# Performance work log

Hardware: AMD Instinct MI355X
Metric: run time of the kernel (lower is better)

## Reference

```python
import jax, jax.numpy as jnp
import numpy as np

HARD_NUM = 700      # hardcoded self.hard_num in HardOIMLoss
OIM_SCALAR = 30.0   # oim_scalar init arg
N, D, P, Q = 4096, 256, 5532, 5000


def _l2norm(x):
    return x / jnp.linalg.norm(x, axis=-1, keepdims=True)


def setup_inputs() -> dict:
    key = jax.random.key(0)
    k1, k2, k3, k4, k5 = jax.random.split(key, 5)
    # OIM features and lookup tables are L2-normalized rows
    inputs = _l2norm(jax.random.normal(k1, (N, D), dtype=jnp.float32))
    lut = _l2norm(jax.random.normal(k2, (P, D), dtype=jnp.float32))
    cq = _l2norm(jax.random.normal(k3, (Q, D), dtype=jnp.float32))
    reliability = jax.random.uniform(k4, (P + Q,), dtype=jnp.float32)
    labels = jax.random.randint(k5, (N,), 0, P, dtype=jnp.int32)
    return {"inputs": inputs, "labels": labels, "lut": lut, "cq": cq,
            "reliability": reliability}


def reference(inputs, labels, lut, cq, reliability):
    # projected[n, c] = <inputs_n, table_c> * reliability_c ;  table = [lut; cq]
    table = jnp.concatenate([lut, cq], axis=0)            # [P+Q, D]
    projected = (inputs @ table.T) * reliability[None, :]  # [N, P+Q]
    C = projected.shape[1]
    # value at sorted-descending index HARD_NUM == (HARD_NUM+1)-th largest
    boundary = jax.lax.top_k(projected, HARD_NUM + 1)[0][:, -1]  # [N]
    hard_mask = projected >= boundary[:, None]
    label_mask = jnp.arange(C, dtype=labels.dtype)[None, :] == labels[:, None]
    mask = hard_mask | label_mask
    logits = jnp.where(mask, projected * OIM_SCALAR, -jnp.inf)
    # cross entropy (mean over rows); label column is always unmasked
    logZ = jax.scipy.special.logsumexp(logits, axis=1)
    tgt = jnp.take_along_axis(logits, labels[:, None].astype(jnp.int32), axis=1)[:, 0]
    return jnp.mean(logZ - tgt)
```

## Files before the change

kernel.cpp:

```cpp
#include <hip/hip_runtime.h>
#include <math.h>

#define N_ROWS 4096
#define DIM    256
#define P_SZ   5532
#define Q_SZ   5000
#define C_COLS 10532
#define TPAD   10624
#define PSTR   10624
#define NGR    (PSTR / 8)
#define K_SEL  701
#define SCALAR 30.0f
#define C2     (SCALAR * 1.4426950408889634f)

typedef __attribute__((ext_vector_type(8))) short   short8;
typedef __attribute__((ext_vector_type(4))) float   float4_t;
typedef __attribute__((ext_vector_type(4))) unsigned short ushort4_t;
typedef __attribute__((ext_vector_type(8))) unsigned short ushort8_t;

__device__ __forceinline__ unsigned short f2bf(float f) {
    unsigned u = __float_as_uint(f);
    unsigned r = u + 0x7FFFu + ((u >> 16) & 1u);
    return (unsigned short)(r >> 16);
}
__device__ __forceinline__ float bf2f(unsigned short u) {
    return __uint_as_float((unsigned)u << 16);
}
__device__ __forceinline__ unsigned key16(unsigned short u) {
    return (u & 0x8000u) ? (unsigned)(~u & 0xFFFFu) : (unsigned)(u | 0x8000u);
}
__device__ __forceinline__ void gload16(const void* g, void* l) {
    __builtin_amdgcn_global_load_lds(
        (const __attribute__((address_space(1))) unsigned int*)g,
        (__attribute__((address_space(3))) unsigned int*)l, 16, 0, 0);
}

#define NIN_G  (N_ROWS * DIM / 4)
#define NTAB_G (TPAD * DIM / 4)

__global__ __launch_bounds__(256) void convert_bf16(
    const float* __restrict__ inputs, const float* __restrict__ lut,
    const float* __restrict__ cq, unsigned short* __restrict__ in_bf,
    unsigned short* __restrict__ tab_bf)
{
    const int g = blockIdx.x * 256 + threadIdx.x;
    if (g >= NIN_G + NTAB_G) return;
    float4_t v;
    unsigned short* dst;
    if (g < NIN_G) {
        v = *(const float4_t*)&inputs[(size_t)g * 4];
        dst = in_bf + (size_t)g * 4;
    } else {
        const int t = g - NIN_G;
        const int row = t >> 6;
        const int c4  = (t & 63) * 4;
        if (row < P_SZ)        v = *(const float4_t*)&lut[(size_t)row * DIM + c4];
        else if (row < C_COLS) v = *(const float4_t*)&cq[(size_t)(row - P_SZ) * DIM + c4];
        else                   v = (float4_t){0.f, 0.f, 0.f, 0.f};
        dst = tab_bf + (size_t)t * 4;
    }
    ushort4_t h = { f2bf(v.x), f2bf(v.y), f2bf(v.z), f2bf(v.w) };
    *(ushort4_t*)dst = h;
}

#define NWG_X 83
#define NWG_Y 32
#define NWG   (NWG_X * NWG_Y)
#define CSTR  132

__global__ __launch_bounds__(256) void gemm_proj(
    const unsigned short* __restrict__ in_bf,
    const unsigned short* __restrict__ tab_bf,
    const float* __restrict__ rel,
    unsigned short* __restrict__ proj)
{
    __shared__ __align__(16) unsigned short smem[128 * CSTR];
    unsigned short* At = smem;
    unsigned short* Bt = smem + 128 * 64;

    const int tid  = threadIdx.x;
    const int lane = tid & 63, wid = tid >> 6;
    const int wm = wid >> 1, wn = wid & 1;

    const int phys = blockIdx.x;
    const int wg   = (phys & 7) * (NWG / 8) + (phys >> 3);
    const int bx   = wg >> 5;
    const int by   = wg & 31;
    const int row0 = by * 128, col0 = bx * 128;

    float4_t acc[4][4];
    #pragma unroll
    for (int i = 0; i < 4; ++i)
        #pragma unroll
        for (int j = 0; j < 4; ++j)
            acc[i][j] = (float4_t){0.f, 0.f, 0.f, 0.f};

    for (int k0 = 0; k0 < DIM; k0 += 64) {
        #pragma unroll
        for (int it = 0; it < 4; ++it) {
            const int g  = it * 256 + tid;
            const int r  = g >> 3;
            const int kb = ((g & 7) * 16) ^ ((r & 7) << 4);
            gload16(in_bf  + (size_t)(row0 + r) * DIM + k0 + (kb >> 1),
                    (char*)At + g * 16);
            gload16(tab_bf + (size_t)(col0 + r) * DIM + k0 + (kb >> 1),
                    (char*)Bt + g * 16);
        }
        __syncthreads();

        #pragma unroll
        for (int kk = 0; kk < 2; ++kk) {
            const int krow = lane & 15;
            const int kb   = kk * 64 + ((lane >> 4) << 4);
            short8 af[4], bfr[4];
            #pragma unroll
            for (int i = 0; i < 4; ++i) {
                const int r = wm * 64 + i * 16 + krow;
                af[i] = *(const short8*)((const char*)At + (r * 128 + (kb ^ ((r & 7) << 4))));
            }
            #pragma unroll
            for (int j = 0; j < 4; ++j) {
                const int r = wn * 64 + j * 16 + krow;
                bfr[j] = *(const short8*)((const char*)Bt + (r * 128 + (kb ^ ((r & 7) << 4))));
            }
            #pragma unroll
            for (int i = 0; i < 4; ++i)
                #pragma unroll
                for (int j = 0; j < 4; ++j)
                    acc[i][j] = __builtin_amdgcn_mfma_f32_16x16x32_bf16(af[i], bfr[j], acc[i][j], 0, 0, 0);
        }
        __syncthreads();
    }

    const int lr = (lane >> 4) << 2;
    const int lc = lane & 15;
    #pragma unroll
    for (int j = 0; j < 4; ++j) {
        const int cl  = wn * 64 + j * 16 + lc;
        const int col = col0 + cl;
        const bool pad = (col >= C_COLS);
        const float rl = pad ? 0.f : rel[col];
        #pragma unroll
        for (int i = 0; i < 4; ++i) {
            const int rbase = wm * 64 + i * 16 + lr;
            #pragma unroll
            for (int rr = 0; rr < 4; ++rr)
                smem[(rbase + rr) * CSTR + cl] =
                    pad ? (unsigned short)0xFF80u : f2bf(acc[i][j][rr] * rl);
        }
    }
    __syncthreads();
    #pragma unroll
    for (int it = 0; it < 8; ++it) {
        const int g = it * 256 + tid;
        const int r = g >> 4;
        const int c8 = (g & 15) * 8;
        *(ushort8_t*)(proj + (size_t)(row0 + r) * PSTR + col0 + c8) =
            *(const ushort8_t*)&smem[r * CSTR + c8];
    }
}

__global__ __launch_bounds__(256) void row_loss_kernel(
    const unsigned short* __restrict__ proj, const int* __restrict__ labels,
    float* __restrict__ row_loss)
{
    __shared__ __align__(16) unsigned short vals[PSTR];
    __shared__ unsigned hist[2048];
    __shared__ unsigned h2[32];
    __shared__ float    e2[32];
    __shared__ unsigned wsum[4];
    __shared__ float    fsum[4];
    __shared__ unsigned sel_bin, sel_k, sel_sub;
    __shared__ float    sel_minor;

    const int tid = threadIdx.x, lane = tid & 63, wid = tid >> 6;
    const int row = blockIdx.x;
    const ushort8_t* prow = (const ushort8_t*)(proj + (size_t)row * PSTR);

    for (int i = tid; i < 2048; i += 256) hist[i] = 0;
    if (tid < 32) { h2[tid] = 0; e2[tid] = 0.f; }
    __syncthreads();

    for (int g = tid; g < NGR; g += 256) {
        const ushort8_t v = prow[g];
        *(ushort8_t*)&vals[g * 8] = v;
        #pragma unroll
        for (int e = 0; e < 8; ++e)
            atomicAdd(&hist[key16(v[e]) >> 5], 1u);
    }
    __syncthreads();

    {
        const int t8 = tid * 8;
        unsigned s = 0;
        #pragma unroll
        for (int b = 0; b < 8; ++b) s += hist[t8 + b];
        unsigned incl = s;
        #pragma unroll
        for (int off = 1; off < 64; off <<= 1) {
            const unsigned t = __shfl_down(incl, off, 64);
            if (lane + off < 64) incl += t;
        }
        if (lane == 0) wsum[wid] = incl;
        __syncthreads();
        unsigned cum = incl - s;
        for (int w = wid + 1; w < 4; ++w) cum += wsum[w];
        #pragma unroll
        for (int b = 7; b >= 0; --b) {
            const unsigned c = hist[t8 + b];
            if (cum < K_SEL && cum + c >= K_SEL) {
                sel_bin = (unsigned)(t8 + b); sel_k = K_SEL - cum;
            }
            cum += c;
        }
    }
    __syncthreads();
    const unsigned b1 = sel_bin;
    const unsigned k2 = sel_k;

    float above = 0.f;
    for (int g = tid; g < NGR; g += 256) {
        const ushort8_t v = *(const ushort8_t*)&vals[g * 8];
        #pragma unroll
        for (int e = 0; e < 8; ++e) {
            const unsigned key = key16(v[e]);
            const unsigned bin = key >> 5;
            if (bin > b1) {
                above += exp2f(C2 * (bf2f(v[e]) - 1.0f));
            } else if (bin == b1) {
                atomicAdd(&h2[key & 31u], 1u);
                atomicAdd(&e2[key & 31u], exp2f(C2 * (bf2f(v[e]) - 1.0f)));
            }
        }
    }
    #pragma unroll
    for (int off = 1; off < 64; off <<= 1) {
        const float t = __shfl_down(above, off, 64);
        if (lane + off < 64) above += t;
    }
    if (lane == 0) fsum[wid] = above;
    __syncthreads();

    if (wid == 0) {
        const unsigned c = (lane < 32) ? h2[lane] : 0u;
        const float    f = (lane < 32) ? e2[lane] : 0.f;
        unsigned ic = c; float fc = f;
        #pragma unroll
        for (int off = 1; off < 64; off <<= 1) {
            const unsigned tc = __shfl_down(ic, off, 64);
            const float    tf = __shfl_down(fc, off, 64);
            if (lane + off < 64) { ic += tc; fc += tf; }
        }
        const unsigned abv = ic - c;
        if (lane < 32 && abv < k2 && abv + c >= k2) {
            sel_sub = (unsigned)lane; sel_minor = fc;
        }
    }
    __syncthreads();

    if (tid == 0) {
        const unsigned bkey = (b1 << 5) | sel_sub;
        float total = fsum[0] + fsum[1] + fsum[2] + fsum[3] + sel_minor;
        const unsigned short ul = vals[labels[row]];
        const float pl = bf2f(ul);
        if (key16(ul) < bkey) total += exp2f(C2 * (pl - 1.0f));
        row_loss[row] = SCALAR * 1.0f + logf(total) - SCALAR * pl;
    }
}

__global__ __launch_bounds__(256) void final_reduce(
    const float* __restrict__ row_loss, float* __restrict__ out)
{
    __shared__ float fred[4];
    const int tid = threadIdx.x, lane = tid & 63, wid = tid >> 6;
    float s = 0.f;
    for (int i = tid; i < N_ROWS; i += 256) s += row_loss[i];
    #pragma unroll
    for (int off = 1; off < 64; off <<= 1) {
        const float t = __shfl_down(s, off, 64);
        if (lane + off < 64) s += t;
    }
    if (lane == 0) fred[wid] = s;
    __syncthreads();
    if (tid == 0) out[0] = (fred[0] + fred[1] + fred[2] + fred[3]) / (float)N_ROWS;
}

extern "C" void kernel_launch(void* const* d_in, const int* in_sizes, int n_in,
                              void* d_out, int out_size, void* d_ws, size_t ws_size,
                              hipStream_t stream) {
    const float* inputs = (const float*)d_in[0];
    const int*   labels = (const int*)d_in[1];
    const float* lut    = (const float*)d_in[2];
    const float* cq     = (const float*)d_in[3];
    const float* rel    = (const float*)d_in[4];
    float* out = (float*)d_out;

    unsigned short* in_bf  = (unsigned short*)d_ws;
    unsigned short* tab_bf = in_bf  + (size_t)N_ROWS * DIM;
    unsigned short* proj   = tab_bf + (size_t)TPAD * DIM;
    float* rl_buf = (float*)(proj + (size_t)N_ROWS * PSTR);

    convert_bf16<<<(NIN_G + NTAB_G) / 256, 256, 0, stream>>>(inputs, lut, cq, in_bf, tab_bf);
    gemm_proj<<<NWG, 256, 0, stream>>>(in_bf, tab_bf, rel, proj);
    row_loss_kernel<<<N_ROWS, 256, 0, stream>>>(proj, labels, rl_buf);
    final_reduce<<<1, 256, 0, stream>>>(rl_buf, out);
}
```

Baseline: 107.4 us.

## Store order-preserving keys, keep row in registers, split histogram across waves

The GEMM epilogue now writes monotone 16-bit sort keys instead of raw bf16 values, so the row-loss kernel no longer applies the key transform per element. The row-loss kernel keeps each thread's row slice in registers instead of staging the whole row in LDS, and it splits the histogram into two copies by wave pair to cut atomic contention. This removes LDS traffic and per-element key math, but raises register pressure (six short8 vectors per thread) and needs an inverse key-to-float conversion before each exp.

```diff
diff --git a/kernel.cpp b/kernel.cpp
--- a/kernel.cpp
+++ b/kernel.cpp
@@ -26,8 +26,13 @@
 __device__ __forceinline__ float bf2f(unsigned short u) {
     return __uint_as_float((unsigned)u << 16);
 }
-__device__ __forceinline__ unsigned key16(unsigned short u) {
-    return (u & 0x8000u) ? (unsigned)(~u & 0xFFFFu) : (unsigned)(u | 0x8000u);
+__device__ __forceinline__ unsigned short key16(unsigned short u) {
+    return (u & 0x8000u) ? (unsigned short)(~u) : (unsigned short)(u | 0x8000u);
+}
+__device__ __forceinline__ float key2f16(unsigned key) {
+    unsigned short b = (key & 0x8000u) ? (unsigned short)(key & 0x7FFFu)
+                                       : (unsigned short)(~key & 0xFFFFu);
+    return bf2f(b);
 }
 __device__ __forceinline__ void gload16(const void* g, void* l) {
     __builtin_amdgcn_global_load_lds(
@@ -146,7 +151,7 @@
             #pragma unroll
             for (int rr = 0; rr < 4; ++rr)
                 smem[(rbase + rr) * CSTR + cl] =
-                    pad ? (unsigned short)0xFF80u : f2bf(acc[i][j][rr] * rl);
+                    pad ? (unsigned short)0u : key16(f2bf(acc[i][j][rr] * rl));
         }
     }
     __syncthreads();
@@ -164,8 +169,7 @@
     const unsigned short* __restrict__ proj, const int* __restrict__ labels,
     float* __restrict__ row_loss)
 {
-    __shared__ __align__(16) unsigned short vals[PSTR];
-    __shared__ unsigned hist[2048];
+    __shared__ unsigned hist[2][2048];
     __shared__ unsigned h2[32];
     __shared__ float    e2[32];
     __shared__ unsigned wsum[4];
@@ -174,27 +178,36 @@
     __shared__ float    sel_minor;
 
     const int tid = threadIdx.x, lane = tid & 63, wid = tid >> 6;
+    const int hsel = wid >> 1;
     const int row = blockIdx.x;
     const ushort8_t* prow = (const ushort8_t*)(proj + (size_t)row * PSTR);
 
-    for (int i = tid; i < 2048; i += 256) hist[i] = 0;
+    for (int i = tid; i < 4096; i += 256) hist[0][i] = 0;
     if (tid < 32) { h2[tid] = 0; e2[tid] = 0.f; }
     __syncthreads();
 
-    for (int g = tid; g < NGR; g += 256) {
-        const ushort8_t v = prow[g];
-        *(ushort8_t*)&vals[g * 8] = v;
-        #pragma unroll
-        for (int e = 0; e < 8; ++e)
-            atomicAdd(&hist[key16(v[e]) >> 5], 1u);
+    ushort8_t r[6];
+    #pragma unroll
+    for (int it = 0; it < 6; ++it) {
+        const int g = it * 256 + tid;
+        if (it < 5 || g < NGR) {
+            r[it] = prow[g];
+            #pragma unroll
+            for (int e = 0; e < 8; ++e)
+                atomicAdd(&hist[hsel][r[it][e] >> 5], 1u);
+        }
     }
     __syncthreads();
 
     {
         const int t8 = tid * 8;
+        unsigned cnt[8];
         unsigned s = 0;
         #pragma unroll
-        for (int b = 0; b < 8; ++b) s += hist[t8 + b];
+        for (int b = 0; b < 8; ++b) {
+            cnt[b] = hist[0][t8 + b] + hist[1][t8 + b];
+            s += cnt[b];
+        }
         unsigned incl = s;
         #pragma unroll
         for (int off = 1; off < 64; off <<= 1) {
@@ -207,7 +220,7 @@
         for (int w = wid + 1; w < 4; ++w) cum += wsum[w];
         #pragma unroll
         for (int b = 7; b >= 0; --b) {
-            const unsigned c = hist[t8 + b];
+            const unsigned c = cnt[b];
             if (cum < K_SEL && cum + c >= K_SEL) {
                 sel_bin = (unsigned)(t8 + b); sel_k = K_SEL - cum;
             }
@@ -217,19 +230,22 @@
     __syncthreads();
     const unsigned b1 = sel_bin;
     const unsigned k2 = sel_k;
+    const unsigned klo = b1 << 5, khi = (b1 + 1) << 5;
 
     float above = 0.f;
-    for (int g = tid; g < NGR; g += 256) {
-        const ushort8_t v = *(const ushort8_t*)&vals[g * 8];
-        #pragma unroll
-        for (int e = 0; e < 8; ++e) {
-            const unsigned key = key16(v[e]);
-            const unsigned bin = key >> 5;
-            if (bin > b1) {
-                above += exp2f(C2 * (bf2f(v[e]) - 1.0f));
-            } else if (bin == b1) {
-                atomicAdd(&h2[key & 31u], 1u);
-                atomicAdd(&e2[key & 31u], exp2f(C2 * (bf2f(v[e]) - 1.0f)));
+    #pragma unroll
+    for (int it = 0; it < 6; ++it) {
+        const int g = it * 256 + tid;
+        if (it < 5 || g < NGR) {
+            #pragma unroll
+            for (int e = 0; e < 8; ++e) {
+                const unsigned key = r[it][e];
+                if (key >= khi) {
+                    above += exp2f(C2 * (key2f16(key) - 1.0f));
+                } else if (key >= klo) {
+                    atomicAdd(&h2[key & 31u], 1u);
+                    atomicAdd(&e2[key & 31u], exp2f(C2 * (key2f16(key) - 1.0f)));
+                }
             }
         }
     }
@@ -261,9 +277,9 @@
     if (tid == 0) {
         const unsigned bkey = (b1 << 5) | sel_sub;
         float total = fsum[0] + fsum[1] + fsum[2] + fsum[3] + sel_minor;
-        const unsigned short ul = vals[labels[row]];
-        const float pl = bf2f(ul);
-        if (key16(ul) < bkey) total += exp2f(C2 * (pl - 1.0f));
+        const unsigned ulk = ((const unsigned short*)prow)[labels[row]];
+        const float pl = key2f16(ulk);
+        if (ulk < bkey) total += exp2f(C2 * (pl - 1.0f));
         row_loss[row] = SCALAR * 1.0f + logf(total) - SCALAR * pl;
     }
 }
```

Measured after the change: 103.5 us. 1.04x faster.
